# Kernel optimization log

Hardware: AMD Instinct MI355X
Metric: run time of the kernel (lower is better)

The kernel has to match this reference:

```python
import math
import jax, jax.numpy as jnp
import numpy as np

NUM_EMBED = 2048
EMBED_FEATS = 64
IN_FEATS = 512
B, T = 16, 4096
COMMITMENT_COST = 0.25


def setup_inputs() -> dict:
    key = jax.random.key(0)
    k1, k2, k3, k4 = jax.random.split(key, 4)
    x = jax.random.normal(k1, (B, IN_FEATS, T), dtype=jnp.float32)
    proj_w = jax.random.normal(k2, (EMBED_FEATS, IN_FEATS), dtype=jnp.float32) / np.sqrt(IN_FEATS)
    proj_b = jax.random.normal(k3, (EMBED_FEATS,), dtype=jnp.float32) * 0.01
    embed = jax.random.normal(k4, (NUM_EMBED, EMBED_FEATS), dtype=jnp.float32)
    return {"x": x, "proj_w": proj_w, "proj_b": proj_b, "embed": embed}


def reference(x, proj_w, proj_b, embed):
    # 1x1 Conv1d projection, then transpose(1,-1): [B, Cin, T] -> [B, T, E]
    h = jnp.einsum('ec,bct->bte', proj_w, x) + proj_b  # [B, T, E]
    Bb, Tt, E = h.shape
    K = embed.shape[0]
    flat = h.reshape(-1, E)  # [N, E]
    # squared distances to codewords: [N, K]
    d2 = (jnp.sum(flat * flat, axis=1, keepdims=True)
          + jnp.sum(embed * embed, axis=1)
          - 2.0 * flat @ embed.T)
    q_idx = jnp.argmin(d2, axis=1)  # [N]
    z_q = embed[q_idx].reshape(Bb, Tt, E)  # one-hot @ embed == gather
    # commitment loss (codebook updated by EMA, so only commitment term)
    commitment = jnp.mean((jax.lax.stop_gradient(z_q) - h) ** 2)
    loss = COMMITMENT_COST * commitment
    # straight-through estimator
    z_q_st = h + jax.lax.stop_gradient(z_q - h)
    # code usage stats
    N = flat.shape[0]
    probs = jnp.zeros((K,), dtype=jnp.float32).at[q_idx].add(1.0) / N
    log_perplexity = -jnp.sum(probs * jnp.log(probs + 1e-10))
    kldiv_r = math.log(K) * (N / Bb) * jnp.ones((Bb, 1), dtype=jnp.float32)
    z_q_out = jnp.swapaxes(z_q_st, 1, 2)  # [B, E, T]
    return z_q_out, loss, kldiv_r, log_perplexity
```

## Files before the change

### kernel.cpp

```cpp
#include <hip/hip_runtime.h>
#include <math.h>

#define B_ 16
#define T_ 4096
#define C_ 512
#define E_ 64
#define K_ 2048
#define N_ (B_*T_)
#define ZQ_ELEMS 4194304

typedef __attribute__((ext_vector_type(8))) short short8;
typedef __attribute__((ext_vector_type(4))) short short4v;
typedef __attribute__((ext_vector_type(4))) float f32x4;

#define WS_EHI   0
#define WS_ELO   262144
#define WS_NHCC  524288
#define WS_WHI   532480
#define WS_WLO   598016
#define WS_HIST  663552
#define WS_LOSS  671744

struct HiLo { short hi, lo; };

__device__ __forceinline__ unsigned short rne16(float v) {
    unsigned u = __float_as_uint(v);
    return (unsigned short)((u + 0x7FFFu + ((u >> 16) & 1u)) >> 16);
}
__device__ __forceinline__ HiLo split_rne(float v) {
    HiLo r;
    unsigned hb = rne16(v);
    r.hi = (short)hb;
    float hf = __uint_as_float((unsigned)hb << 16);
    r.lo = (short)rne16(v - hf);
    return r;
}

typedef const __attribute__((address_space(1))) void* gas1_t;
typedef __attribute__((address_space(3))) void* las3_t;
__device__ __forceinline__ void gl16(const void* g, void* l) {
    __builtin_amdgcn_global_load_lds((gas1_t)g, (las3_t)l, 16, 0, 0);
}

__global__ void prep_kernel(const float* __restrict__ embed,
                            const float* __restrict__ W,
                            short* __restrict__ ehi, short* __restrict__ elo,
                            float* __restrict__ nhcc,
                            short* __restrict__ whi, short* __restrict__ wlo) {
    const int tid = threadIdx.x;
    if (blockIdx.x < 64) {
        const int row = blockIdx.x * 32 + (tid >> 3);
        const int g = tid & 7;
        const float* src = embed + (size_t)row * 64 + g * 8;
        short8 hv, lv;
        float s = 0.f;
#pragma unroll
        for (int j = 0; j < 8; ++j) {
            float v = src[j];
            s = fmaf(v, v, s);
            HiLo r = split_rne(v);
            hv[j] = r.hi; lv[j] = r.lo;
        }
        const int c128 = row >> 7, r = row & 127;
        const int kt = r >> 4, col = r & 15, ks = g >> 2, qe = g & 3;
        const int slot = (kt * 2 + ks) * 64 + qe * 16 + col;
        *(short8*)(ehi + c128 * 8192 + slot * 8) = hv;
        *(short8*)(elo + c128 * 8192 + slot * 8) = lv;
        s += __shfl_xor(s, 1, 64);
        s += __shfl_xor(s, 2, 64);
        s += __shfl_xor(s, 4, 64);
        if (g == 0) nhcc[row] = -0.5f * s;
    } else {
        int idx = ((blockIdx.x - 64) * 256 + tid) * 4;
        float4 v = *(const float4*)(W + idx);
        short4v h, l;
        HiLo a = split_rne(v.x); h[0] = a.hi; l[0] = a.lo;
        HiLo b = split_rne(v.y); h[1] = b.hi; l[1] = b.lo;
        HiLo c = split_rne(v.z); h[2] = c.hi; l[2] = c.lo;
        HiLo d = split_rne(v.w); h[3] = d.hi; l[3] = d.lo;
        *(short4v*)(whi + idx) = h;
        *(short4v*)(wlo + idx) = l;
    }
}

__global__ __launch_bounds__(512, 4) void projvq_kernel(
        const float* __restrict__ x,
        const short* __restrict__ whi, const short* __restrict__ wlo,
        const float* __restrict__ bias,
        const short* __restrict__ ehi, const short* __restrict__ elo,
        const float* __restrict__ nhcc,
        const float* __restrict__ embed, float* __restrict__ out,
        int* __restrict__ hist, float* __restrict__ lossacc) {
    __shared__ __align__(16) char smem[68096];
    float* xsf  = (float*)smem;
    short* es   = (short*)smem;
    short* aimg = (short*)(smem + 32768);
    float* ccs  = (float*)(smem + 65536);
    int*   qsm  = (int*)(smem + 66560);
    float* vtmp = (float*)(smem + 67072);
    int*   itmp = (int*)(smem + 67584);
    float* tile = (float*)smem;

    const int tid = threadIdx.x;
    const int wave = tid >> 6, lane = tid & 63;
    const int row16 = lane & 15, quad = lane >> 4;
    const int b  = blockIdx.x >> 5;
    const int t0 = (blockIdx.x & 31) * 128;
    const float* xb = x + (size_t)b * C_ * T_ + t0;

    f32x4 cc = *(const f32x4*)(nhcc + tid * 4);

    f32x4 acc[4];
#pragma unroll
    for (int et = 0; et < 4; ++et) acc[et] = (f32x4){0.f, 0.f, 0.f, 0.f};

#pragma unroll
    for (int j = 0; j < 2; ++j) {
        int o = j * 512 + tid;
        gl16(xb + (size_t)(o >> 5) * T_ + (o & 31) * 4, xsf + o * 4);
    }
    __syncthreads();

    for (int it = 0; it < 16; ++it) {
        const int c0 = it * 32;
        const int p = it & 1;
        if (it < 15) {
#pragma unroll
            for (int j = 0; j < 2; ++j) {
                int o = j * 512 + tid;
                gl16(xb + (size_t)(c0 + 32 + (o >> 5)) * T_ + (o & 31) * 4,
                     xsf + (p ^ 1) * 4096 + o * 4);
            }
        }
        const float* xsb = xsf + p * 4096;
        short8 bh, bl;
#pragma unroll
        for (int j = 0; j < 8; ++j) {
            float v = xsb[(quad * 8 + j) * 128 + wave * 16 + row16];
            HiLo r = split_rne(v);
            bh[j] = r.hi; bl[j] = r.lo;
        }
#pragma unroll
        for (int et = 0; et < 4; ++et) {
            size_t aoff = (size_t)(et * 16 + row16) * C_ + c0 + quad * 8;
            short8 ah = *(const short8*)(whi + aoff);
            short8 al = *(const short8*)(wlo + aoff);
            acc[et] = __builtin_amdgcn_mfma_f32_16x16x32_bf16(ah, bh, acc[et], 0, 0, 0);
            acc[et] = __builtin_amdgcn_mfma_f32_16x16x32_bf16(al, bh, acc[et], 0, 0, 0);
            acc[et] = __builtin_amdgcn_mfma_f32_16x16x32_bf16(ah, bl, acc[et], 0, 0, 0);
            acc[et] = __builtin_amdgcn_mfma_f32_16x16x32_bf16(al, bl, acc[et], 0, 0, 0);
        }
        __syncthreads();
    }

#pragma unroll
    for (int j = 0; j < 2; ++j) {
        int o = (j * 512 + tid) * 8;
        gl16(ehi + o, es + o);
        gl16(elo + o, es + 8192 + o);
    }

    float hh = 0.f;
#pragma unroll
    for (int et = 0; et < 4; ++et) {
        float4 bv = *(const float4*)(bias + et * 16 + quad * 4);
        f32x4 a = acc[et];
        a[0] += bv.x; a[1] += bv.y; a[2] += bv.z; a[3] += bv.w;
        hh = fmaf(a[0], a[0], hh); hh = fmaf(a[1], a[1], hh);
        hh = fmaf(a[2], a[2], hh); hh = fmaf(a[3], a[3], hh);
        short4v hv, lv;
#pragma unroll
        for (int r = 0; r < 4; ++r) {
            HiLo sp = split_rne(a[r]);
            hv[r] = sp.hi; lv[r] = sp.lo;
        }
        const int ks = et >> 1;
        const int qe = (et & 1) * 2 + (quad >> 1);
        const int j0 = (quad & 1) * 4;
        const int sl = ((wave * 2 + ks) * 64 + qe * 16 + row16) * 8 + j0;
        *(short4v*)(aimg + sl) = hv;
        *(short4v*)(aimg + 8192 + sl) = lv;
    }
#pragma unroll
    for (int m = 1; m < 64; m <<= 1) hh += __shfl_xor(hh, m, 64);
    if (lane == 0) atomicAdd(lossacc, hh);
    __syncthreads();

    const int pair = wave & 3, kh = wave >> 2;
    short8 a_hi[2][2], a_lo[2][2];
#pragma unroll
    for (int rt = 0; rt < 2; ++rt)
#pragma unroll
        for (int ks = 0; ks < 2; ++ks) {
            int sl = (((2 * pair + rt) * 2 + ks) * 64 + lane) * 8;
            a_hi[rt][ks] = *(const short8*)(aimg + sl);
            a_lo[rt][ks] = *(const short8*)(aimg + 8192 + sl);
        }
    if ((tid >> 5) == 0) *(f32x4*)(ccs + (tid & 31) * 4) = cc;
    __syncthreads();

    float vmax[2][4];
    int   vidx[2][4];
#pragma unroll
    for (int rt = 0; rt < 2; ++rt)
#pragma unroll
        for (int rg = 0; rg < 4; ++rg) { vmax[rt][rg] = -3.4e38f; vidx[rt][rg] = 0; }

    for (int c = 0; c < 16; ++c) {
        if (c < 15) {
            const short* sh  = ehi + (c + 1) * 8192;
            const short* sl2 = elo + (c + 1) * 8192;
            short* dst = es + ((c + 1) & 1) * 16384;
#pragma unroll
            for (int j = 0; j < 2; ++j) {
                int o = (j * 512 + tid) * 8;
                gl16(sh + o, dst + o);
                gl16(sl2 + o, dst + 8192 + o);
            }
            if ((tid >> 5) == c + 1)
                *(f32x4*)(ccs + ((c + 1) & 1) * 128 + (tid & 31) * 4) = cc;
        }
        const short* eb = es + (c & 1) * 16384;
        const float* cb = ccs + (c & 1) * 128;
#pragma unroll
        for (int k4 = 0; k4 < 4; ++k4) {
            const int kt = kh * 4 + k4;
            const float ci = cb[kt * 16 + row16];
            const short* pb = eb + kt * 1024;
            short8 bh0 = *(const short8*)(pb + lane * 8);
            short8 bh1 = *(const short8*)(pb + 512 + lane * 8);
            short8 bl0 = *(const short8*)(pb + 8192 + lane * 8);
            short8 bl1 = *(const short8*)(pb + 8192 + 512 + lane * 8);
            const int kk = c * 128 + kt * 16 + row16;
#pragma unroll
            for (int rt = 0; rt < 2; ++rt) {
                f32x4 a2 = (f32x4){0.f, 0.f, 0.f, 0.f};
                a2 = __builtin_amdgcn_mfma_f32_16x16x32_bf16(a_hi[rt][0], bh0, a2, 0, 0, 0);
                a2 = __builtin_amdgcn_mfma_f32_16x16x32_bf16(a_hi[rt][1], bh1, a2, 0, 0, 0);
                a2 = __builtin_amdgcn_mfma_f32_16x16x32_bf16(a_lo[rt][0], bh0, a2, 0, 0, 0);
                a2 = __builtin_amdgcn_mfma_f32_16x16x32_bf16(a_lo[rt][1], bh1, a2, 0, 0, 0);
                a2 = __builtin_amdgcn_mfma_f32_16x16x32_bf16(a_hi[rt][0], bl0, a2, 0, 0, 0);
                a2 = __builtin_amdgcn_mfma_f32_16x16x32_bf16(a_hi[rt][1], bl1, a2, 0, 0, 0);
#pragma unroll
                for (int rg = 0; rg < 4; ++rg) {
                    float v = a2[rg] + ci;
                    if (v > vmax[rt][rg]) { vmax[rt][rg] = v; vidx[rt][rg] = kk; }
                }
            }
        }
        __syncthreads();
    }

    float s = 0.f;
#pragma unroll
    for (int rt = 0; rt < 2; ++rt)
#pragma unroll
        for (int rg = 0; rg < 4; ++rg) {
            float v = vmax[rt][rg];
            int ix = vidx[rt][rg];
#pragma unroll
            for (int m = 1; m < 16; m <<= 1) {
                float ov = __shfl_xor(v, m, 64);
                int   oi = __shfl_xor(ix, m, 64);
                if (ov > v || (ov == v && oi < ix)) { v = ov; ix = oi; }
            }
            vmax[rt][rg] = v; vidx[rt][rg] = ix;
        }
    if (kh == 1 && row16 == 0) {
#pragma unroll
        for (int rt = 0; rt < 2; ++rt)
#pragma unroll
            for (int rg = 0; rg < 4; ++rg) {
                const int row = (2 * pair + rt) * 16 + quad * 4 + rg;
                vtmp[row] = vmax[rt][rg];
                itmp[row] = vidx[rt][rg];
            }
    }
    __syncthreads();
    if (kh == 0) {
        if (row16 == 0) {
#pragma unroll
            for (int rt = 0; rt < 2; ++rt)
#pragma unroll
                for (int rg = 0; rg < 4; ++rg) {
                    const int row = (2 * pair + rt) * 16 + quad * 4 + rg;
                    float v = vmax[rt][rg];
                    int ix = vidx[rt][rg];
                    const float ov = vtmp[row];
                    const int   oi = itmp[row];
                    if (ov > v || (ov == v && oi < ix)) { v = ov; ix = oi; }
                    qsm[row] = ix;
                    atomicAdd(&hist[ix], 1);
                    s += v;
                }
        }
        s += __shfl_xor(s, 16, 64);
        s += __shfl_xor(s, 32, 64);
        if (lane == 0) atomicAdd(lossacc, -2.f * s);
    }
    __syncthreads();

    {
        const int r = tid >> 2, piece = tid & 3;
        const float* src = embed + (size_t)qsm[r] * 64 + piece * 16;
        float* dst = tile + r * 69 + piece * 16;
#pragma unroll
        for (int j = 0; j < 4; ++j)
            *(float4*)(dst + j * 4) = *(const float4*)(src + j * 4);
    }
    __syncthreads();
    {
        const int tt = tid & 63;
        const int eo = tid >> 6;
        float* ob = out + ((size_t)b * 64) * T_ + t0;
#pragma unroll
        for (int j = 0; j < 8; ++j) {
            const int e = j * 8 + eo;
            ob[(size_t)e * T_ + tt]      = tile[tt * 69 + e];
            ob[(size_t)e * T_ + 64 + tt] = tile[(tt + 64) * 69 + e];
        }
    }
}

__global__ void finalize_kernel(const int* __restrict__ hist,
                                const float* __restrict__ lossacc,
                                float* __restrict__ out) {
    __shared__ float red[4];
    const int tid = threadIdx.x;
    float s = 0.f;
    for (int k = tid; k < K_; k += 256) {
        float p = (float)hist[k] * (1.f / 65536.f);
        s -= p * logf(p + 1e-10f);
    }
#pragma unroll
    for (int m = 1; m < 64; m <<= 1) s += __shfl_xor(s, m, 64);
    if ((tid & 63) == 0) red[tid >> 6] = s;
    __syncthreads();
    if (tid == 0) {
        float lp = red[0] + red[1] + red[2] + red[3];
        out[ZQ_ELEMS] = 0.25f * lossacc[0] / (float)ZQ_ELEMS;
        out[ZQ_ELEMS + 17] = lp;
    }
    if (tid < 16) out[ZQ_ELEMS + 1 + tid] = logf(2048.f) * 4096.f;
}

extern "C" void kernel_launch(void* const* d_in, const int* in_sizes, int n_in,
                              void* d_out, int out_size, void* d_ws, size_t ws_size,
                              hipStream_t stream) {
    const float* x      = (const float*)d_in[0];
    const float* proj_w = (const float*)d_in[1];
    const float* proj_b = (const float*)d_in[2];
    const float* embed  = (const float*)d_in[3];
    float* out = (float*)d_out;
    char* ws = (char*)d_ws;

    short* e_hi = (short*)(ws + WS_EHI);
    short* e_lo = (short*)(ws + WS_ELO);
    float* nhcc = (float*)(ws + WS_NHCC);
    short* w_hi = (short*)(ws + WS_WHI);
    short* w_lo = (short*)(ws + WS_WLO);
    int*   hist = (int*)(ws + WS_HIST);
    float* lossac = (float*)(ws + WS_LOSS);

    (void)hipMemsetAsync(ws + WS_HIST, 0, K_ * sizeof(int) + sizeof(float), stream);

    prep_kernel<<<96, 256, 0, stream>>>(embed, proj_w, e_hi, e_lo, nhcc, w_hi, w_lo);
    projvq_kernel<<<N_ / 128, 512, 0, stream>>>(x, w_hi, w_lo, proj_b,
                                                e_hi, e_lo, nhcc, embed, out,
                                                hist, lossac);
    finalize_kernel<<<1, 256, 0, stream>>>(hist, lossac, out);
}
```

Before: 309.8 us.

## Split fused projection+VQ kernel into separate projection and VQ kernels

Replaces the single fused projection-plus-codebook-search kernel with two kernels. The first does the 1x1 conv projection using 1024 smaller blocks with double-buffered x loads and writes h as a bf16 hi/lo register image to workspace. The second loads that image and runs the codebook distance search, argmin, histogram and output write. The aim is more parallelism and better occupancy for the projection phase, at the cost of an extra global round trip for h and one more launch; the fused kernel stays as a fallback when the workspace is too small.

```diff
diff --git a/kernel.cpp b/kernel.cpp
--- a/kernel.cpp
+++ b/kernel.cpp
@@ -20,6 +20,8 @@
 #define WS_WLO   598016
 #define WS_HIST  663552
 #define WS_LOSS  671744
+#define WS_HIMG  1048576
+#define WS_NEED  (WS_HIMG + 512*16384*2)
 
 struct HiLo { short hi, lo; };
 
@@ -83,6 +85,262 @@
     }
 }
 
+__global__ __launch_bounds__(256, 4) void proj_kernel(
+        const float* __restrict__ x,
+        const short* __restrict__ whi, const short* __restrict__ wlo,
+        const float* __restrict__ bias,
+        short* __restrict__ himg, float* __restrict__ lossacc) {
+    __shared__ __align__(16) float xsf[2][2048];
+
+    const int tid = threadIdx.x;
+    const int wave = tid >> 6, lane = tid & 63;
+    const int row16 = lane & 15, quad = lane >> 4;
+    const int blk = blockIdx.x;
+    const int b  = blk >> 6;
+    const int t0 = (blk & 63) * 64;
+    const float* xb = x + (size_t)b * C_ * T_ + t0;
+
+    f32x4 acc[4];
+#pragma unroll
+    for (int et = 0; et < 4; ++et) acc[et] = (f32x4){0.f, 0.f, 0.f, 0.f};
+
+#pragma unroll
+    for (int j = 0; j < 2; ++j) {
+        int o = j * 256 + tid;
+        int tsrc = ((o & 15) * 4) ^ (((o >> 7) & 1) << 4);
+        gl16(xb + (size_t)(o >> 4) * T_ + tsrc, &xsf[0][o * 4]);
+    }
+    __syncthreads();
+
+    for (int it = 0; it < 16; ++it) {
+        const int c0 = it * 32;
+        const int p = it & 1;
+        if (it < 15) {
+#pragma unroll
+            for (int j = 0; j < 2; ++j) {
+                int o = j * 256 + tid;
+                int tsrc = ((o & 15) * 4) ^ (((o >> 7) & 1) << 4);
+                gl16(xb + (size_t)(c0 + 32 + (o >> 4)) * T_ + tsrc,
+                     &xsf[p ^ 1][o * 4]);
+            }
+        }
+        const float* xsb = xsf[p];
+        const int tsw = (wave * 16 + row16) ^ ((quad & 1) << 4);
+        short8 bh, bl;
+#pragma unroll
+        for (int j = 0; j < 8; ++j) {
+            float v = xsb[(quad * 8 + j) * 64 + tsw];
+            HiLo r = split_rne(v);
+            bh[j] = r.hi; bl[j] = r.lo;
+        }
+#pragma unroll
+        for (int et = 0; et < 4; ++et) {
+            size_t aoff = (size_t)(et * 16 + row16) * C_ + c0 + quad * 8;
+            short8 ah = *(const short8*)(whi + aoff);
+            short8 al = *(const short8*)(wlo + aoff);
+            acc[et] = __builtin_amdgcn_mfma_f32_16x16x32_bf16(ah, bh, acc[et], 0, 0, 0);
+            acc[et] = __builtin_amdgcn_mfma_f32_16x16x32_bf16(al, bh, acc[et], 0, 0, 0);
+            acc[et] = __builtin_amdgcn_mfma_f32_16x16x32_bf16(ah, bl, acc[et], 0, 0, 0);
+            acc[et] = __builtin_amdgcn_mfma_f32_16x16x32_bf16(al, bl, acc[et], 0, 0, 0);
+        }
+        __syncthreads();
+    }
+
+    short* gb = himg + (size_t)(blk >> 1) * 16384;
+    const int w2 = (blk & 1) * 4 + wave;
+    float hh = 0.f;
+#pragma unroll
+    for (int et = 0; et < 4; ++et) {
+        float4 bv = *(const float4*)(bias + et * 16 + quad * 4);
+        f32x4 a = acc[et];
+        a[0] += bv.x; a[1] += bv.y; a[2] += bv.z; a[3] += bv.w;
+        hh = fmaf(a[0], a[0], hh); hh = fmaf(a[1], a[1], hh);
+        hh = fmaf(a[2], a[2], hh); hh = fmaf(a[3], a[3], hh);
+        short4v hv, lv;
+#pragma unroll
+        for (int r = 0; r < 4; ++r) {
+            HiLo sp = split_rne(a[r]);
+            hv[r] = sp.hi; lv[r] = sp.lo;
+        }
+        const int ks = et >> 1;
+        const int qe = (et & 1) * 2 + (quad >> 1);
+        const int j0 = (quad & 1) * 4;
+        const int sl = ((w2 * 2 + ks) * 64 + qe * 16 + row16) * 8 + j0;
+        *(short4v*)(gb + sl) = hv;
+        *(short4v*)(gb + 8192 + sl) = lv;
+    }
+#pragma unroll
+    for (int m = 1; m < 64; m <<= 1) hh += __shfl_xor(hh, m, 64);
+    if (lane == 0) atomicAdd(lossacc, hh);
+}
+
+__global__ __launch_bounds__(512, 4) void vq_kernel(
+        const short* __restrict__ himg,
+        const short* __restrict__ ehi, const short* __restrict__ elo,
+        const float* __restrict__ nhcc,
+        const float* __restrict__ embed, float* __restrict__ out,
+        int* __restrict__ hist, float* __restrict__ lossacc) {
+    __shared__ __align__(16) char smem[68096];
+    short* es   = (short*)smem;
+    float* ccs  = (float*)(smem + 65536);
+    int*   qsm  = (int*)(smem + 66560);
+    float* vtmp = (float*)(smem + 67072);
+    int*   itmp = (int*)(smem + 67584);
+    float* tile = (float*)smem;
+
+    const int tid = threadIdx.x;
+    const int wave = tid >> 6, lane = tid & 63;
+    const int row16 = lane & 15, quad = lane >> 4;
+    const int g = blockIdx.x;
+    const int b  = g >> 5;
+    const int t0 = (g & 31) * 128;
+
+    f32x4 cc = *(const f32x4*)(nhcc + tid * 4);
+
+    const short* gb = himg + (size_t)g * 16384;
+    const int pair = wave & 3, kh = wave >> 2;
+    short8 a_hi[2][2], a_lo[2][2];
+#pragma unroll
+    for (int rt = 0; rt < 2; ++rt)
+#pragma unroll
+        for (int ks = 0; ks < 2; ++ks) {
+            int sl = (((2 * pair + rt) * 2 + ks) * 64 + lane) * 8;
+            a_hi[rt][ks] = *(const short8*)(gb + sl);
+            a_lo[rt][ks] = *(const short8*)(gb + 8192 + sl);
+        }
+
+#pragma unroll
+    for (int j = 0; j < 2; ++j) {
+        int o = (j * 512 + tid) * 8;
+        gl16(ehi + o, es + o);
+        gl16(elo + o, es + 8192 + o);
+    }
+    if ((tid >> 5) == 0) *(f32x4*)(ccs + (tid & 31) * 4) = cc;
+    __syncthreads();
+
+    float vmax[2][4];
+    int   vidx[2][4];
+#pragma unroll
+    for (int rt = 0; rt < 2; ++rt)
+#pragma unroll
+        for (int rg = 0; rg < 4; ++rg) { vmax[rt][rg] = -3.4e38f; vidx[rt][rg] = 0; }
+
+    for (int c = 0; c < 16; ++c) {
+        if (c < 15) {
+            const short* sh  = ehi + (c + 1) * 8192;
+            const short* sl2 = elo + (c + 1) * 8192;
+            short* dst = es + ((c + 1) & 1) * 16384;
+#pragma unroll
+            for (int j = 0; j < 2; ++j) {
+                int o = (j * 512 + tid) * 8;
+                gl16(sh + o, dst + o);
+                gl16(sl2 + o, dst + 8192 + o);
+            }
+            if ((tid >> 5) == c + 1)
+                *(f32x4*)(ccs + ((c + 1) & 1) * 128 + (tid & 31) * 4) = cc;
+        }
+        const short* eb = es + (c & 1) * 16384;
+        const float* cb = ccs + (c & 1) * 128;
+#pragma unroll
+        for (int k4 = 0; k4 < 4; ++k4) {
+            const int kt = kh * 4 + k4;
+            const float ci = cb[kt * 16 + row16];
+            const short* pb = eb + kt * 1024;
+            short8 bh0 = *(const short8*)(pb + lane * 8);
+            short8 bh1 = *(const short8*)(pb + 512 + lane * 8);
+            short8 bl0 = *(const short8*)(pb + 8192 + lane * 8);
+            short8 bl1 = *(const short8*)(pb + 8192 + 512 + lane * 8);
+            const int kk = c * 128 + kt * 16 + row16;
+#pragma unroll
+            for (int rt = 0; rt < 2; ++rt) {
+                f32x4 a2 = (f32x4){0.f, 0.f, 0.f, 0.f};
+                a2 = __builtin_amdgcn_mfma_f32_16x16x32_bf16(a_hi[rt][0], bh0, a2, 0, 0, 0);
+                a2 = __builtin_amdgcn_mfma_f32_16x16x32_bf16(a_hi[rt][1], bh1, a2, 0, 0, 0);
+                a2 = __builtin_amdgcn_mfma_f32_16x16x32_bf16(a_lo[rt][0], bh0, a2, 0, 0, 0);
+                a2 = __builtin_amdgcn_mfma_f32_16x16x32_bf16(a_lo[rt][1], bh1, a2, 0, 0, 0);
+                a2 = __builtin_amdgcn_mfma_f32_16x16x32_bf16(a_hi[rt][0], bl0, a2, 0, 0, 0);
+                a2 = __builtin_amdgcn_mfma_f32_16x16x32_bf16(a_hi[rt][1], bl1, a2, 0, 0, 0);
+#pragma unroll
+                for (int rg = 0; rg < 4; ++rg) {
+                    float v = a2[rg] + ci;
+                    if (v > vmax[rt][rg]) { vmax[rt][rg] = v; vidx[rt][rg] = kk; }
+                }
+            }
+        }
+        __syncthreads();
+    }
+
+    float s = 0.f;
+#pragma unroll
+    for (int rt = 0; rt < 2; ++rt)
+#pragma unroll
+        for (int rg = 0; rg < 4; ++rg) {
+            float v = vmax[rt][rg];
+            int ix = vidx[rt][rg];
+#pragma unroll
+            for (int m = 1; m < 16; m <<= 1) {
+                float ov = __shfl_xor(v, m, 64);
+                int   oi = __shfl_xor(ix, m, 64);
+                if (ov > v || (ov == v && oi < ix)) { v = ov; ix = oi; }
+            }
+            vmax[rt][rg] = v; vidx[rt][rg] = ix;
+        }
+    if (kh == 1 && row16 == 0) {
+#pragma unroll
+        for (int rt = 0; rt < 2; ++rt)
+#pragma unroll
+            for (int rg = 0; rg < 4; ++rg) {
+                const int row = (2 * pair + rt) * 16 + quad * 4 + rg;
+                vtmp[row] = vmax[rt][rg];
+                itmp[row] = vidx[rt][rg];
+            }
+    }
+    __syncthreads();
+    if (kh == 0) {
+        if (row16 == 0) {
+#pragma unroll
+            for (int rt = 0; rt < 2; ++rt)
+#pragma unroll
+                for (int rg = 0; rg < 4; ++rg) {
+                    const int row = (2 * pair + rt) * 16 + quad * 4 + rg;
+                    float v = vmax[rt][rg];
+                    int ix = vidx[rt][rg];
+                    const float ov = vtmp[row];
+                    const int   oi = itmp[row];
+                    if (ov > v || (ov == v && oi < ix)) { v = ov; ix = oi; }
+                    qsm[row] = ix;
+                    atomicAdd(&hist[ix], 1);
+                    s += v;
+                }
+        }
+        s += __shfl_xor(s, 16, 64);
+        s += __shfl_xor(s, 32, 64);
+        if (lane == 0) atomicAdd(lossacc, -2.f * s);
+    }
+    __syncthreads();
+
+    {
+        const int r = tid >> 2, piece = tid & 3;
+        const float* src = embed + (size_t)qsm[r] * 64 + piece * 16;
+        float* dst = tile + r * 69 + piece * 16;
+#pragma unroll
+        for (int j = 0; j < 4; ++j)
+            *(float4*)(dst + j * 4) = *(const float4*)(src + j * 4);
+    }
+    __syncthreads();
+    {
+        const int tt = tid & 63;
+        const int eo = tid >> 6;
+        float* ob = out + ((size_t)b * 64) * T_ + t0;
+#pragma unroll
+        for (int j = 0; j < 8; ++j) {
+            const int e = j * 8 + eo;
+            ob[(size_t)e * T_ + tt]      = tile[tt * 69 + e];
+            ob[(size_t)e * T_ + 64 + tt] = tile[(tt + 64) * 69 + e];
+        }
+    }
+}
+
 __global__ __launch_bounds__(512, 4) void projvq_kernel(
         const float* __restrict__ x,
         const short* __restrict__ whi, const short* __restrict__ wlo,
@@ -361,12 +619,19 @@
     short* w_lo = (short*)(ws + WS_WLO);
     int*   hist = (int*)(ws + WS_HIST);
     float* lossac = (float*)(ws + WS_LOSS);
+    short* himg = (short*)(ws + WS_HIMG);
 
     (void)hipMemsetAsync(ws + WS_HIST, 0, K_ * sizeof(int) + sizeof(float), stream);
 
     prep_kernel<<<96, 256, 0, stream>>>(embed, proj_w, e_hi, e_lo, nhcc, w_hi, w_lo);
-    projvq_kernel<<<N_ / 128, 512, 0, stream>>>(x, w_hi, w_lo, proj_b,
-                                                e_hi, e_lo, nhcc, embed, out,
-                                                hist, lossac);
+    if (ws_size >= (size_t)WS_NEED) {
+        proj_kernel<<<1024, 256, 0, stream>>>(x, w_hi, w_lo, proj_b, himg, lossac);
+        vq_kernel<<<512, 512, 0, stream>>>(himg, e_hi, e_lo, nhcc, embed, out,
+                                           hist, lossac);
+    } else {
+        projvq_kernel<<<N_ / 128, 512, 0, stream>>>(x, w_hi, w_lo, proj_b,
+                                                    e_hi, e_lo, nhcc, embed, out,
+                                                    hist, lossac);
+    }
     finalize_kernel<<<1, 256, 0, stream>>>(hist, lossac, out);
 }
```

New measurement: 344.4 us. 11.2% more time.
